# Performance work log

Hardware: AMD Instinct MI355X
Metric: run time of the kernel (lower is better)

Reference implementation:

```python
import jax, jax.numpy as jnp
import numpy as np
from jax import lax

ALPHA = 1.5
N_ITER = 100


def entmax(z, alpha=ALPHA, n_iter=N_ITER):
    # z: [B, Sq, Sk] scores. Bisection for the entmax threshold tau.
    z = (alpha - 1.0) * z.astype(jnp.float32)
    S = z.shape[-1]
    z_max = jnp.max(z, axis=-1, keepdims=True)          # [B, Sq, 1]
    tau_min = z_max - 1.0
    tau_max = z_max - np.float32(S ** (1.0 - alpha))
    inv = 1.0 / (alpha - 1.0)                            # = 2.0 for alpha=1.5

    def body(carry, _):
        tmin, tmax, _ = carry
        tau = (tmin + tmax) * 0.5
        p = jnp.maximum(z - tau, 0.0) ** inv             # [B, Sq, Sk]
        Z = jnp.sum(p, axis=-1, keepdims=True)           # [B, Sq, 1]
        tmin = jnp.where(Z >= 1.0, tau, tmin)
        tmax = jnp.where(Z < 1.0, tau, tmax)
        return (tmin, tmax, tau), None

    init = (tau_min, tau_max, (tau_min + tau_max) * 0.5)
    (tmin, tmax, tau), _ = lax.scan(jax.checkpoint(body), init, None, length=n_iter)
    # faithful to the TF code: final output uses p, Z from the LAST iteration's tau
    p = jnp.maximum(z - tau, 0.0) ** inv
    Z = jnp.sum(p, axis=-1, keepdims=True)
    return p / Z


def setup_inputs() -> dict:
    key = jax.random.key(0)
    kq, kk, kv = jax.random.split(key, 3)
    B, S, D = 8, 2048, 128
    return {
        "query": jax.random.normal(kq, (B, S, D), dtype=jnp.float32),
        "key": jax.random.normal(kk, (B, S, D), dtype=jnp.float32),
        "value": jax.random.normal(kv, (B, S, D), dtype=jnp.float32),
    }


def reference(query, key, value):
    scores = jnp.einsum("bqd,bkd->bqk", query, key)      # QK^T, no scaling (as in source)
    weights = entmax(scores, alpha=ALPHA, n_iter=N_ITER)
    return jnp.einsum("bqk,bkd->bqd", weights, value)
```

## Files before the change

kernel.cpp:

```cpp
#include <hip/hip_runtime.h>

#define BB 8
#define SS 2048
#define DD 128
#define ROWS 16
#define NW 8
#define CTW 16

typedef short bf16x8 __attribute__((ext_vector_type(8)));
typedef float f32x4 __attribute__((ext_vector_type(4)));

template <int I> struct IC { static constexpr int value = I; };
template <int I, int N, typename F>
__device__ __forceinline__ void sfor(F&& f) {
  if constexpr (I < N) { f(IC<I>{}); sfor<I + 1, N>((F&&)f); }
}

__device__ __forceinline__ short f2bf(float x) {
  return __builtin_bit_cast(short, (__bf16)x);
}
__device__ __forceinline__ float bf2f(short u) {
  return __uint_as_float(((unsigned)(unsigned short)u) << 16);
}

__global__ __launch_bounds__(256)
void ksplit(const float* __restrict__ K, short* __restrict__ Khi) {
  const int lin  = blockIdx.x * 256 + threadIdx.x;
  const int b    = lin >> 15;
  const int rem  = lin & 32767;
  const int ct   = rem >> 8;
  const int s    = (rem >> 6) & 3;
  const int lane = rem & 63;
  const int quad = lane >> 4, m16 = lane & 15;
  const size_t elem = (size_t)(b * SS + ct * 16 + m16) * DD + s * 32 + quad * 8;
  const float4 v0 = *(const float4*)(K + elem);
  const float4 v1 = *(const float4*)(K + elem + 4);
  const float f[8] = {v0.x, v0.y, v0.z, v0.w, v1.x, v1.y, v1.z, v1.w};
  bf16x8 h;
#pragma unroll
  for (int e = 0; e < 8; ++e) h[e] = f2bf(f[e]);
  *(bf16x8*)(Khi + (size_t)lin * 8) = h;
}

__global__ __launch_bounds__(512) __attribute__((amdgpu_waves_per_eu(4)))
void attn(const float* __restrict__ Q, const short* __restrict__ Khi,
          const float* __restrict__ K, const float* __restrict__ V,
          float* __restrict__ Out) {
  __shared__ unsigned short Qs[ROWS][136];
  __shared__ float rbuf[ROWS][64];
  __shared__ int   scol[ROWS][64];
  __shared__ float exM[NW][ROWS];
  __shared__ float exZ[NW][ROWS];
  __shared__ int   rcnt[ROWS];
  __shared__ float tauB[ROWS], ZB[ROWS];
  __shared__ int   flagv;
  __shared__ float obuf[ROWS][DD];

  const int tid  = threadIdx.x;
  const int lane = tid & 63;
  const int wid  = __builtin_amdgcn_readfirstlane(tid >> 6);
  const int quad = lane >> 4, m16 = lane & 15;
  const int b    = blockIdx.x & 7;
  const int qt   = blockIdx.x >> 3;

  const float* Qb = Q + (size_t)(b * SS + qt * ROWS) * DD;
  const float* Kb = K + (size_t)b * SS * DD;
  const float* Vb = V + (size_t)b * SS * DD;
  float*       Ob = Out + (size_t)(b * SS + qt * ROWS) * DD;
  const short* KHb = Khi + (size_t)b * SS * DD;

  if (tid < ROWS) rcnt[tid] = 0;
  if (tid == ROWS) flagv = 0;

  {
    const int row = tid >> 5, d = (tid & 31) * 4;
    const float4 v = *(const float4*)&Qb[row * DD + d];
    ushort4 h;
    h.x = (unsigned short)f2bf(0.5f * v.x);
    h.y = (unsigned short)f2bf(0.5f * v.y);
    h.z = (unsigned short)f2bf(0.5f * v.z);
    h.w = (unsigned short)f2bf(0.5f * v.w);
    *(ushort4*)&Qs[row][d] = h;
  }
  __syncthreads();

  bf16x8 qh[4];
#pragma unroll
  for (int s = 0; s < 4; ++s)
    qh[s] = *(const bf16x8*)&Qs[m16][s * 32 + quad * 8];

  f32x4 acc[CTW];
  sfor<0, CTW>([&](auto ic) {
    constexpr int i = ic.value;
    const int ct = wid * CTW + i;
    const short* bh0 = KHb + ((size_t)ct << 11) + lane * 8;
    f32x4 c = {0.f, 0.f, 0.f, 0.f};
    sfor<0, 4>([&](auto sc) {
      constexpr int s = sc.value;
      const bf16x8 bh = *(const bf16x8*)(bh0 + (s << 9));
      c = __builtin_amdgcn_mfma_f32_16x16x32_bf16(qh[s], bh, c, 0, 0, 0);
    });
    acc[i] = c;
  });

  float mx[4] = {-1e38f, -1e38f, -1e38f, -1e38f};
  sfor<0, CTW>([&](auto ic) {
#pragma unroll
    for (int j = 0; j < 4; ++j) mx[j] = fmaxf(mx[j], acc[ic.value][j]);
  });
#pragma unroll
  for (int j = 0; j < 4; ++j)
#pragma unroll
    for (int s = 1; s <= 8; s <<= 1) mx[j] = fmaxf(mx[j], __shfl_xor(mx[j], s));
  if (m16 == 0) {
#pragma unroll
    for (int j = 0; j < 4; ++j) exM[wid][4 * quad + j] = mx[j];
  }
  __syncthreads();
  float M4[4];
#pragma unroll
  for (int j = 0; j < 4; ++j) {
    float m = -1e38f;
#pragma unroll
    for (int w = 0; w < NW; ++w) m = fmaxf(m, exM[w][4 * quad + j]);
    M4[j] = m;
  }

  sfor<0, CTW>([&](auto ic) {
    constexpr int i = ic.value;
    const int col = wid * 256 + i * 16 + m16;
#pragma unroll
    for (int j = 0; j < 4; ++j) {
      const int row = 4 * quad + j;
      if (acc[i][j] > M4[j] - 1.25f) {
        const int pos = atomicAdd(&rcnt[row], 1);
        if (pos < 64) { scol[row][pos] = col; rbuf[row][pos] = acc[i][j]; }
        else atomicOr(&flagv, 1);
      }
    }
  });
  __syncthreads();

  if (flagv == 0) {
#pragma unroll
    for (int rr = 0; rr < 2; ++rr) {
      const int row = 2 * wid + rr;
      const int n = rcnt[row];
      const float2 q2 = *(const float2*)&Qb[row * DD + lane * 2];
      for (int i = 0; i < n; ++i) {
        const int c = scol[row][i];
        const float2 k2 = *(const float2*)&Kb[(size_t)c * DD + lane * 2];
        float t = fmaf(q2.x, k2.x, q2.y * k2.y);
#pragma unroll
        for (int s = 1; s <= 32; s <<= 1) t += __shfl_xor(t, s);
        if (lane == 0) rbuf[row][i] = 0.5f * t;
      }
    }
  }
  __syncthreads();

  float tau4[4], Z4[4];
  if (flagv == 0) {
    const int row = lane >> 2;
    const int n = rcnt[row];
    float cv[16];
#pragma unroll
    for (int k = 0; k < 16; ++k) {
      const int i = (lane & 3) + 4 * k;
      cv[k] = (i < n) ? rbuf[row][i] : -1e38f;
    }
    float Mr = cv[0];
#pragma unroll
    for (int k = 1; k < 16; ++k) Mr = fmaxf(Mr, cv[k]);
    Mr = fmaxf(Mr, __shfl_xor(Mr, 1));
    Mr = fmaxf(Mr, __shfl_xor(Mr, 2));
    float tmn = Mr - 1.0f, tmx = Mr - 0.022097086912079608f;
    float tau = 0.5f * (tmn + tmx), Zr = 0.f;
    for (int it = 0; it < 100; ++it) {
      tau = 0.5f * (tmn + tmx);
      float z0 = 0.f, z1 = 0.f, z2 = 0.f, z3 = 0.f;
#pragma unroll
      for (int k = 0; k < 16; k += 4) {
        const float t0 = fmaxf(cv[k + 0] - tau, 0.f); z0 = fmaf(t0, t0, z0);
        const float t1 = fmaxf(cv[k + 1] - tau, 0.f); z1 = fmaf(t1, t1, z1);
        const float t2 = fmaxf(cv[k + 2] - tau, 0.f); z2 = fmaf(t2, t2, z2);
        const float t3 = fmaxf(cv[k + 3] - tau, 0.f); z3 = fmaf(t3, t3, z3);
      }
      float zp = (z0 + z1) + (z2 + z3);
      zp += __shfl_xor(zp, 1);
      zp += __shfl_xor(zp, 2);
      Zr = zp;
      const float nmn = (zp >= 1.f) ? tau : tmn;
      const float nmx = (zp >= 1.f) ? tmx : tau;
      const bool ch = (nmn != tmn) || (nmx != tmx);
      tmn = nmn; tmx = nmx;
      if (!__any(ch)) break;
    }
    if (wid == 0 && (lane & 3) == 0) { tauB[row] = tau; ZB[row] = Zr; }
  } else {
    float tmn4[4], tmx4[4];
#pragma unroll
    for (int j = 0; j < 4; ++j) {
      tmn4[j] = M4[j] - 1.0f; tmx4[j] = M4[j] - 0.022097086912079608f;
      tau4[j] = 0.5f * (tmn4[j] + tmx4[j]); Z4[j] = 0.f;
    }
    for (int it = 0; it < 100; ++it) {
      float zp[4] = {0.f, 0.f, 0.f, 0.f};
#pragma unroll
      for (int j = 0; j < 4; ++j) tau4[j] = 0.5f * (tmn4[j] + tmx4[j]);
      sfor<0, CTW>([&](auto ic) {
#pragma unroll
        for (int j = 0; j < 4; ++j) {
          const float tt = fmaxf(acc[ic.value][j] - tau4[j], 0.f);
          zp[j] = fmaf(tt, tt, zp[j]);
        }
      });
#pragma unroll
      for (int j = 0; j < 4; ++j)
#pragma unroll
        for (int s = 1; s <= 8; s <<= 1) zp[j] += __shfl_xor(zp[j], s);
      if (m16 == 0) {
#pragma unroll
        for (int j = 0; j < 4; ++j) exZ[wid][4 * quad + j] = zp[j];
      }
      __syncthreads();
      bool ch = false;
#pragma unroll
      for (int j = 0; j < 4; ++j) {
        float Zf = 0.f;
#pragma unroll
        for (int w = 0; w < NW; ++w) Zf += exZ[w][4 * quad + j];
        Z4[j] = Zf;
        const float nmn = (Zf >= 1.f) ? tau4[j] : tmn4[j];
        const float nmx = (Zf >= 1.f) ? tmx4[j] : tau4[j];
        ch = ch || (nmn != tmn4[j]) || (nmx != tmx4[j]);
        tmn4[j] = nmn; tmx4[j] = nmx;
      }
      __syncthreads();
      if (!ch) break;
    }
  }
  __syncthreads();

  if (flagv == 0) {
#pragma unroll
    for (int rr = 0; rr < 2; ++rr) {
      const int row = 2 * wid + rr;
      const int n = rcnt[row];
      const float tau = tauB[row];
      const float iz  = 1.0f / ZB[row];
      float2 o = {0.f, 0.f};
      for (int i = 0; i < n; ++i) {
        const float rv = rbuf[row][i];
        const float tt = fmaxf(rv - tau, 0.f);
        const float pi = tt * tt * iz;
        const int   c  = scol[row][i];
        const float2 v2 = *(const float2*)&Vb[(size_t)c * DD + lane * 2];
        o.x = fmaf(pi, v2.x, o.x);
        o.y = fmaf(pi, v2.y, o.y);
      }
      *(float2*)&Ob[row * DD + lane * 2] = o;
    }
  } else {
    for (int i = tid; i < ROWS * DD; i += 512) ((float*)obuf)[i] = 0.f;
    __syncthreads();
    sfor<0, CTW>([&](auto ic) {
      constexpr int i = ic.value;
      const int col = wid * 256 + i * 16 + m16;
#pragma unroll
      for (int j = 0; j < 4; ++j) {
        const int row = 4 * quad + j;
        const float tt = fmaxf(acc[i][j] - tau4[j], 0.f);
        const float p = tt * tt / Z4[j];
        if (p > 0.f) {
          for (int d = 0; d < DD; ++d)
            atomicAdd(&obuf[row][d], p * Vb[(size_t)col * DD + d]);
        }
      }
    });
    __syncthreads();
    for (int i = tid; i < ROWS * DD; i += 512) {
      const int row = i >> 7, d = i & 127;
      Ob[row * DD + d] = obuf[row][d];
    }
  }
}

extern "C" void kernel_launch(void* const* d_in, const int* in_sizes, int n_in,
                              void* d_out, int out_size, void* d_ws, size_t ws_size,
                              hipStream_t stream) {
  const float* Q = (const float*)d_in[0];
  const float* K = (const float*)d_in[1];
  const float* V = (const float*)d_in[2];
  float* out = (float*)d_out;
  short* Khi = (short*)d_ws;

  hipLaunchKernelGGL(ksplit, dim3(BB * SS * DD / (256 * 8)), dim3(256), 0, stream,
                     K, Khi);
  hipLaunchKernelGGL(attn, dim3(BB * (SS / ROWS)), dim3(512), 0, stream,
                     Q, Khi, K, V, out);
}
```

Before: 142.5 us.

## Double-buffer K tiles through LDS with async loads and restructure per-row bisection

```diff
diff --git a/kernel.cpp b/kernel.cpp
--- a/kernel.cpp
+++ b/kernel.cpp
@@ -21,6 +21,15 @@
 }
 __device__ __forceinline__ float bf2f(short u) {
   return __uint_as_float(((unsigned)(unsigned short)u) << 16);
+}
+
+__device__ __forceinline__ void stage_tile(const short* g, short* l) {
+#pragma unroll
+  for (int s = 0; s < 4; ++s) {
+    __builtin_amdgcn_global_load_lds(
+        (const __attribute__((address_space(1))) void*)(g + (s << 9)),
+        (__attribute__((address_space(3))) void*)(l + (s << 9)), 16, 0, 0);
+  }
 }
 
 __global__ __launch_bounds__(256)
@@ -46,6 +55,7 @@
 void attn(const float* __restrict__ Q, const short* __restrict__ Khi,
           const float* __restrict__ K, const float* __restrict__ V,
           float* __restrict__ Out) {
+  __shared__ short kring[NW][2][2048];
   __shared__ unsigned short Qs[ROWS][136];
   __shared__ float rbuf[ROWS][64];
   __shared__ int   scol[ROWS][64];
@@ -54,7 +64,6 @@
   __shared__ int   rcnt[ROWS];
   __shared__ float tauB[ROWS], ZB[ROWS];
   __shared__ int   flagv;
-  __shared__ float obuf[ROWS][DD];
 
   const int tid  = threadIdx.x;
   const int lane = tid & 63;
@@ -89,18 +98,30 @@
   for (int s = 0; s < 4; ++s)
     qh[s] = *(const bf16x8*)&Qs[m16][s * 32 + quad * 8];
 
+  short* ring0 = &kring[wid][0][0];
+  short* ring1 = &kring[wid][1][0];
+  const short* gw = KHb + ((size_t)(wid * CTW) << 11) + lane * 8;
+
+  stage_tile(gw + 0 * 2048, ring0);
+  stage_tile(gw + 1 * 2048, ring1);
+
   f32x4 acc[CTW];
   sfor<0, CTW>([&](auto ic) {
     constexpr int i = ic.value;
-    const int ct = wid * CTW + i;
-    const short* bh0 = KHb + ((size_t)ct << 11) + lane * 8;
+    if constexpr (i < CTW - 1) asm volatile("s_waitcnt vmcnt(4)" ::: "memory");
+    else                       asm volatile("s_waitcnt vmcnt(0)" ::: "memory");
+    const short* sbl = ((i & 1) ? ring1 : ring0) + lane * 8;
     f32x4 c = {0.f, 0.f, 0.f, 0.f};
     sfor<0, 4>([&](auto sc) {
       constexpr int s = sc.value;
-      const bf16x8 bh = *(const bf16x8*)(bh0 + (s << 9));
+      const bf16x8 bh = *(const bf16x8*)(sbl + (s << 9));
       c = __builtin_amdgcn_mfma_f32_16x16x32_bf16(qh[s], bh, c, 0, 0, 0);
     });
     acc[i] = c;
+    if constexpr (i + 2 < CTW) {
+      asm volatile("s_waitcnt lgkmcnt(0)" ::: "memory");
+      stage_tile(gw + (i + 2) * 2048, (i & 1) ? ring1 : ring0);
+    }
   });
 
   float mx[4] = {-1e38f, -1e38f, -1e38f, -1e38f};
@@ -142,6 +163,7 @@
   __syncthreads();
 
   if (flagv == 0) {
+
 #pragma unroll
     for (int rr = 0; rr < 2; ++rr) {
       const int row = 2 * wid + rr;
@@ -156,93 +178,36 @@
         if (lane == 0) rbuf[row][i] = 0.5f * t;
       }
     }
-  }
-  __syncthreads();
-
-  float tau4[4], Z4[4];
-  if (flagv == 0) {
-    const int row = lane >> 2;
-    const int n = rcnt[row];
-    float cv[16];
-#pragma unroll
-    for (int k = 0; k < 16; ++k) {
-      const int i = (lane & 3) + 4 * k;
-      cv[k] = (i < n) ? rbuf[row][i] : -1e38f;
-    }
-    float Mr = cv[0];
-#pragma unroll
-    for (int k = 1; k < 16; ++k) Mr = fmaxf(Mr, cv[k]);
-    Mr = fmaxf(Mr, __shfl_xor(Mr, 1));
-    Mr = fmaxf(Mr, __shfl_xor(Mr, 2));
-    float tmn = Mr - 1.0f, tmx = Mr - 0.022097086912079608f;
-    float tau = 0.5f * (tmn + tmx), Zr = 0.f;
-    for (int it = 0; it < 100; ++it) {
-      tau = 0.5f * (tmn + tmx);
-      float z0 = 0.f, z1 = 0.f, z2 = 0.f, z3 = 0.f;
-#pragma unroll
-      for (int k = 0; k < 16; k += 4) {
-        const float t0 = fmaxf(cv[k + 0] - tau, 0.f); z0 = fmaf(t0, t0, z0);
-        const float t1 = fmaxf(cv[k + 1] - tau, 0.f); z1 = fmaf(t1, t1, z1);
-        const float t2 = fmaxf(cv[k + 2] - tau, 0.f); z2 = fmaf(t2, t2, z2);
-        const float t3 = fmaxf(cv[k + 3] - tau, 0.f); z3 = fmaf(t3, t3, z3);
-      }
-      float zp = (z0 + z1) + (z2 + z3);
-      zp += __shfl_xor(zp, 1);
-      zp += __shfl_xor(zp, 2);
-      Zr = zp;
-      const float nmn = (zp >= 1.f) ? tau : tmn;
-      const float nmx = (zp >= 1.f) ? tmx : tau;
-      const bool ch = (nmn != tmn) || (nmx != tmx);
-      tmn = nmn; tmx = nmx;
-      if (!__any(ch)) break;
-    }
-    if (wid == 0 && (lane & 3) == 0) { tauB[row] = tau; ZB[row] = Zr; }
-  } else {
-    float tmn4[4], tmx4[4];
-#pragma unroll
-    for (int j = 0; j < 4; ++j) {
-      tmn4[j] = M4[j] - 1.0f; tmx4[j] = M4[j] - 0.022097086912079608f;
-      tau4[j] = 0.5f * (tmn4[j] + tmx4[j]); Z4[j] = 0.f;
-    }
-    for (int it = 0; it < 100; ++it) {
-      float zp[4] = {0.f, 0.f, 0.f, 0.f};
-#pragma unroll
-      for (int j = 0; j < 4; ++j) tau4[j] = 0.5f * (tmn4[j] + tmx4[j]);
-      sfor<0, CTW>([&](auto ic) {
-#pragma unroll
-        for (int j = 0; j < 4; ++j) {
-          const float tt = fmaxf(acc[ic.value][j] - tau4[j], 0.f);
-          zp[j] = fmaf(tt, tt, zp[j]);
-        }
-      });
-#pragma unroll
-      for (int j = 0; j < 4; ++j)
-#pragma unroll
-        for (int s = 1; s <= 8; s <<= 1) zp[j] += __shfl_xor(zp[j], s);
-      if (m16 == 0) {
-#pragma unroll
-        for (int j = 0; j < 4; ++j) exZ[wid][4 * quad + j] = zp[j];
-      }
-      __syncthreads();
-      bool ch = false;
-#pragma unroll
-      for (int j = 0; j < 4; ++j) {
-        float Zf = 0.f;
-#pragma unroll
-        for (int w = 0; w < NW; ++w) Zf += exZ[w][4 * quad + j];
-        Z4[j] = Zf;
-        const float nmn = (Zf >= 1.f) ? tau4[j] : tmn4[j];
-        const float nmx = (Zf >= 1.f) ? tmx4[j] : tau4[j];
-        ch = ch || (nmn != tmn4[j]) || (nmx != tmx4[j]);
-        tmn4[j] = nmn; tmx4[j] = nmx;
-      }
-      __syncthreads();
-      if (!ch) break;
-    }
-  }
-  __syncthreads();
-
-  if (flagv == 0) {
+
+    {
+      const int rr32 = lane >> 5;
+      const int row  = 2 * wid + rr32;
+      const int l32  = lane & 31;
+      const int n = rcnt[row];
+      const float a0 = (l32 < n)      ? rbuf[row][l32]      : -1e38f;
+      const float a1 = (l32 + 32 < n) ? rbuf[row][l32 + 32] : -1e38f;
+      float Mr = fmaxf(a0, a1);
+#pragma unroll
+      for (int s = 1; s <= 16; s <<= 1) Mr = fmaxf(Mr, __shfl_xor(Mr, s));
+      float tmn = Mr - 1.0f, tmx = Mr - 0.022097086912079608f;
+      float tau = 0.5f * (tmn + tmx), Zr = 0.f;
+      for (int it = 0; it < 100; ++it) {
+        tau = 0.5f * (tmn + tmx);
+        const float t0 = fmaxf(a0 - tau, 0.f);
+        const float t1 = fmaxf(a1 - tau, 0.f);
+        float zp = fmaf(t0, t0, t1 * t1);
+#pragma unroll
+        for (int s = 1; s <= 16; s <<= 1) zp += __shfl_xor(zp, s);
+        Zr = zp;
+        const float nmn = (zp >= 1.f) ? tau : tmn;
+        const float nmx = (zp >= 1.f) ? tmx : tau;
+        const bool ch = (nmn != tmn) || (nmx != tmx);
+        tmn = nmn; tmx = nmx;
+        if (!__any(ch)) break;
+      }
+      if (l32 == 0) { tauB[row] = tau; ZB[row] = Zr; }
+    }
+
 #pragma unroll
     for (int rr = 0; rr < 2; ++rr) {
       const int row = 2 * wid + rr;
@@ -262,6 +227,50 @@
       *(float2*)&Ob[row * DD + lane * 2] = o;
     }
   } else {
+    float tau4[4], Z4[4];
+    float tmn4[4], tmx4[4];
+#pragma unroll
+    for (int j = 0; j < 4; ++j) {
+      tmn4[j] = M4[j] - 1.0f; tmx4[j] = M4[j] - 0.022097086912079608f;
+      tau4[j] = 0.5f * (tmn4[j] + tmx4[j]); Z4[j] = 0.f;
+    }
+    for (int it = 0; it < 100; ++it) {
+      float zp[4] = {0.f, 0.f, 0.f, 0.f};
+#pragma unroll
+      for (int j = 0; j < 4; ++j) tau4[j] = 0.5f * (tmn4[j] + tmx4[j]);
+      sfor<0, CTW>([&](auto ic) {
+#pragma unroll
+        for (int j = 0; j < 4; ++j) {
+          const float tt = fmaxf(acc[ic.value][j] - tau4[j], 0.f);
+          zp[j] = fmaf(tt, tt, zp[j]);
+        }
+      });
+#pragma unroll
+      for (int j = 0; j < 4; ++j)
+#pragma unroll
+        for (int s = 1; s <= 8; s <<= 1) zp[j] += __shfl_xor(zp[j], s);
+      if (m16 == 0) {
+#pragma unroll
+        for (int j = 0; j < 4; ++j) exZ[wid][4 * quad + j] = zp[j];
+      }
+      __syncthreads();
+      bool ch = false;
+#pragma unroll
+      for (int j = 0; j < 4; ++j) {
+        float Zf = 0.f;
+#pragma unroll
+        for (int w = 0; w < NW; ++w) Zf += exZ[w][4 * quad + j];
+        Z4[j] = Zf;
+        const float nmn = (Zf >= 1.f) ? tau4[j] : tmn4[j];
+        const float nmx = (Zf >= 1.f) ? tmx4[j] : tau4[j];
+        ch = ch || (nmn != tmn4[j]) || (nmx != tmx4[j]);
+        tmn4[j] = nmn; tmx4[j] = nmx;
+      }
+      __syncthreads();
+      if (!ch) break;
+    }
+
+    float (*obuf)[DD] = (float (*)[DD])&kring[0][0][0];
     for (int i = tid; i < ROWS * DD; i += 512) ((float*)obuf)[i] = 0.f;
     __syncthreads();
     sfor<0, CTW>([&](auto ic) {
```

After: 137.4 us. 3.6% less time.
